# Performance work log

Hardware: AMD Instinct MI355X
Metric: run time of the kernel (lower is better)

## Reference

```python
import jax, jax.numpy as jnp
import numpy as np
from jax import lax

FEAT_STRIDE = 16
PRE_NMS_TOP_N = 6000   # cfg['TEST'].RPN_PRE_NMS_TOP_N
POST_NMS_TOP_N = 300   # cfg['TEST'].RPN_POST_NMS_TOP_N
NMS_THRESH = 0.7       # cfg['TEST'].RPN_NMS_THRESH
MIN_SIZE = 16.0        # cfg['TEST'].RPN_MIN_SIZE
B, A, H, W = 32, 9, 128, 128
NEG_INF = jnp.float32(-1e30)


def _whctrs(a):
    w = a[2] - a[0] + 1.0
    h = a[3] - a[1] + 1.0
    return w, h, a[0] + 0.5 * (w - 1), a[1] + 0.5 * (h - 1)

def _mkanchors(ws, hs, xc, yc):
    ws = ws[:, None]; hs = hs[:, None]
    return np.hstack((xc - 0.5 * (ws - 1), yc - 0.5 * (hs - 1),
                      xc + 0.5 * (ws - 1), yc + 0.5 * (hs - 1)))

def _ratio_enum(anchor, ratios):
    w, h, xc, yc = _whctrs(anchor)
    size = w * h
    ws = np.round(np.sqrt(size / ratios))
    hs = np.round(ws * ratios)
    return _mkanchors(ws, hs, xc, yc)

def _scale_enum(anchor, scales):
    w, h, xc, yc = _whctrs(anchor)
    return _mkanchors(w * scales, h * scales, xc, yc)

def generate_anchors(base_size=16, ratios=np.array([0.5, 1.0, 2.0]), scales=np.array([8.0, 16.0, 32.0])):
    base = np.array([1, 1, base_size, base_size], dtype=np.float64) - 1
    ra = _ratio_enum(base, ratios)
    return np.vstack([_scale_enum(ra[i], scales) for i in range(ra.shape[0])]).astype(np.float32)

_BASE_ANCHORS = generate_anchors()  # (A, 4)

def _all_anchors(h, w):
    sx = np.arange(w) * FEAT_STRIDE
    sy = np.arange(h) * FEAT_STRIDE
    sx, sy = np.meshgrid(sx, sy)  # row-major (h, w) matches permute(0,2,3,1) ordering
    shifts = np.stack([sx.ravel(), sy.ravel(), sx.ravel(), sy.ravel()], axis=1).astype(np.float32)
    return jnp.asarray((shifts[:, None, :] + _BASE_ANCHORS[None, :, :]).reshape(-1, 4))  # (h*w*A, 4)

# ---- bbox_transform_inv / clip_boxes ----

def _decode(anchors, deltas):
    ws = anchors[:, 2] - anchors[:, 0] + 1.0
    hs = anchors[:, 3] - anchors[:, 1] + 1.0
    cx = anchors[:, 0] + 0.5 * ws
    cy = anchors[:, 1] + 0.5 * hs
    dx, dy, dw, dh = deltas[:, 0], deltas[:, 1], deltas[:, 2], deltas[:, 3]
    pcx = dx * ws + cx
    pcy = dy * hs + cy
    pw = jnp.exp(dw) * ws
    ph = jnp.exp(dh) * hs
    return jnp.stack([pcx - 0.5 * pw, pcy - 0.5 * ph, pcx + 0.5 * pw, pcy + 0.5 * ph], axis=1)

def _clip(b, imh, imw):
    x1 = jnp.clip(b[:, 0], 0.0, imw - 1.0)
    y1 = jnp.clip(b[:, 1], 0.0, imh - 1.0)
    x2 = jnp.clip(b[:, 2], 0.0, imw - 1.0)
    y2 = jnp.clip(b[:, 3], 0.0, imh - 1.0)
    return jnp.stack([x1, y1, x2, y2], axis=1)

# ---- greedy NMS: pick top-score box, suppress IoU > thresh, repeat POST times ----

def _nms_select(boxes, scores):
    # boxes: (PRE, 4) score-sorted; scores: (PRE,)
    areas = (boxes[:, 2] - boxes[:, 0] + 1.0) * (boxes[:, 3] - boxes[:, 1] + 1.0)

    def body(i, st):
        s, keep, valid = st
        j = jnp.argmax(s)
        keep = keep.at[i].set(j)
        valid = valid.at[i].set(s[j] > NEG_INF)
        b = boxes[j]
        xx1 = jnp.maximum(b[0], boxes[:, 0])
        yy1 = jnp.maximum(b[1], boxes[:, 1])
        xx2 = jnp.minimum(b[2], boxes[:, 2])
        yy2 = jnp.minimum(b[3], boxes[:, 3])
        inter = jnp.maximum(xx2 - xx1 + 1.0, 0.0) * jnp.maximum(yy2 - yy1 + 1.0, 0.0)
        iou = inter / jnp.maximum(areas[j] + areas - inter, 1e-6)
        s = jnp.where(iou > NMS_THRESH, NEG_INF, s)  # suppresses j itself (IoU = 1)
        return s, keep, valid

    init = (scores, jnp.zeros((POST_NMS_TOP_N,), jnp.int32), jnp.zeros((POST_NMS_TOP_N,), bool))
    _, keep, valid = lax.fori_loop(0, POST_NMS_TOP_N, body, init)
    return keep, valid

def _per_image(sc, dl, info, anchors):
    prop = _clip(_decode(anchors, dl), info[0], info[1])  # (K*A, 4)
    ws = prop[:, 2] - prop[:, 0] + 1.0
    hs = prop[:, 3] - prop[:, 1] + 1.0
    min_sz = MIN_SIZE * info[2]
    sc = jnp.where((ws >= min_sz) & (hs >= min_sz), sc, NEG_INF)
    top_s, top_i = lax.top_k(sc, PRE_NMS_TOP_N)
    cand = prop[top_i]  # (PRE, 4)
    keep, valid = _nms_select(cand, top_s)
    return cand[keep] * valid[:, None].astype(cand.dtype)  # zero-pad invalid rows

def _forward(rpn_cls_prob, rpn_bbox_pred, im_info):
    b, _, h, w = rpn_cls_prob.shape
    anchors = _all_anchors(h, w)
    scores = rpn_cls_prob[:, A:, :, :].transpose(0, 2, 3, 1).reshape(b, -1)  # (b, h*w*A)
    deltas = rpn_bbox_pred.transpose(0, 2, 3, 1).reshape(b, -1, 4)           # (b, h*w*A, 4)
    boxes = jax.vmap(lambda s, d, i: _per_image(s, d, i, anchors))(scores, deltas, im_info)
    ids = jnp.broadcast_to(jnp.arange(b, dtype=boxes.dtype)[:, None, None], (b, POST_NMS_TOP_N, 1))
    return jnp.concatenate([ids, boxes], axis=2)  # (b, POST, 5): [batch_idx, x1, y1, x2, y2]

def setup_inputs() -> dict:
    key = jax.random.key(0)
    k1, k2 = jax.random.split(key)
    rpn_cls_prob = jax.random.uniform(k1, (B, 2 * A, H, W), dtype=jnp.float32)
    rpn_bbox_pred = jax.random.normal(k2, (B, 4 * A, H, W), dtype=jnp.float32) * 0.2
    im_info = jnp.tile(jnp.array([[H * FEAT_STRIDE, W * FEAT_STRIDE, 1.0]], dtype=jnp.float32), (B, 1))
    return {"rpn_cls_prob": rpn_cls_prob, "rpn_bbox_pred": rpn_bbox_pred, "im_info": im_info}

def reference(rpn_cls_prob, rpn_bbox_pred, im_info):
    return _forward(rpn_cls_prob, rpn_bbox_pred, im_info)
```

## Files before the change

kernel.cpp:

```cpp
#include <hip/hip_runtime.h>
#include <cstdint>
#include <cstddef>

#pragma clang fp contract(off)

typedef unsigned long long u64;

#define NB 32
#define NA 9
#define NH 128
#define NW 128
#define HW (NH*NW)
#define NANCH (NA*HW)
#define PRE_N 6000
#define POST_N 300
#define CAND_CAP 8192
#define NMS_T 0.7f
#define GX_GATHER 24

__constant__ float c_wa[9] = {184.f,368.f,736.f,128.f,256.f,512.f,88.f,176.f,352.f};
__constant__ float c_ha[9] = {96.f,192.f,384.f,128.f,256.f,512.f,176.f,352.f,704.f};

__device__ __forceinline__ float4 decode_clip(int a, int h, int w,
    float dx, float dy, float dlw, float dlh, float imh, float imw) {
  float wa = c_wa[a], ha = c_ha[a];
  float cx = (float)w * 16.0f + 8.0f;
  float cy = (float)h * 16.0f + 8.0f;
  float pcx = dx * wa + cx;
  float pcy = dy * ha + cy;
  float pw = expf(dlw) * wa;
  float ph = expf(dlh) * ha;
  float x1 = pcx - 0.5f * pw;
  float y1 = pcy - 0.5f * ph;
  float x2 = pcx + 0.5f * pw;
  float y2 = pcy + 0.5f * ph;
  float4 r;
  r.x = fminf(fmaxf(x1, 0.0f), imw - 1.0f);
  r.y = fminf(fmaxf(y1, 0.0f), imh - 1.0f);
  r.z = fminf(fmaxf(x2, 0.0f), imw - 1.0f);
  r.w = fminf(fmaxf(y2, 0.0f), imh - 1.0f);
  return r;
}

__device__ __forceinline__ unsigned score_key(float sc, float bw, float bh, float msz) {
  unsigned bits = __float_as_uint(sc);
  unsigned key = (bits & 0x80000000u) ? ~bits : (bits | 0x80000000u);
  if (!(bw >= msz && bh >= msz)) key = 0u;
  return key;
}

__device__ __forceinline__ bool sup_test4(float4 v, float ar, float4 p, float pa) {
  float xx1 = fmaxf(p.x, v.x), yy1 = fmaxf(p.y, v.y);
  float xx2 = fminf(p.z, v.z), yy2 = fminf(p.w, v.w);
  float iw = fmaxf(xx2 - xx1 + 1.0f, 0.0f);
  float ih = fmaxf(yy2 - yy1 + 1.0f, 0.0f);
  float inter = iw * ih;
  float iou = inter / fmaxf(pa + ar - inter, 1e-6f);
  return iou > NMS_T;
}

__global__ __launch_bounds__(256) void k_keys(const float* __restrict__ cls,
    const float* __restrict__ dl, const float* __restrict__ info,
    unsigned* __restrict__ keys, unsigned* __restrict__ hist) {
  __shared__ unsigned hsh[4096];
  int tid = threadIdx.x;
  for (int i = tid; i < 4096; i += 256) hsh[i] = 0;
  int t = blockIdx.x * 256 + tid;
  int b = blockIdx.y;
  int hw0 = t * 4;
  int h = hw0 >> 7;
  const float* dlb  = dl  + (size_t)b * (4*NA*HW);
  const float* clsb = cls + (size_t)b * (2*NA*HW);
  float imh = info[b*3+0], imw = info[b*3+1];
  float msz = 16.0f * info[b*3+2];
  unsigned* kb = keys + (size_t)b * NANCH;
  __syncthreads();
  #pragma unroll
  for (int a = 0; a < 9; ++a) {
    float4 dx4 = *(const float4*)&dlb[(a*4+0)*HW + hw0];
    float4 dy4 = *(const float4*)&dlb[(a*4+1)*HW + hw0];
    float4 dw4 = *(const float4*)&dlb[(a*4+2)*HW + hw0];
    float4 dh4 = *(const float4*)&dlb[(a*4+3)*HW + hw0];
    float4 sc4 = *(const float4*)&clsb[(NA+a)*HW + hw0];
    uint4 out;
    {
      float4 bx = decode_clip(a, h, (hw0+0)&127, dx4.x, dy4.x, dw4.x, dh4.x, imh, imw);
      out.x = score_key(sc4.x, bx.z-bx.x+1.0f, bx.w-bx.y+1.0f, msz);
    }
    {
      float4 bx = decode_clip(a, h, (hw0+1)&127, dx4.y, dy4.y, dw4.y, dh4.y, imh, imw);
      out.y = score_key(sc4.y, bx.z-bx.x+1.0f, bx.w-bx.y+1.0f, msz);
    }
    {
      float4 bx = decode_clip(a, h, (hw0+2)&127, dx4.z, dy4.z, dw4.z, dh4.z, imh, imw);
      out.z = score_key(sc4.z, bx.z-bx.x+1.0f, bx.w-bx.y+1.0f, msz);
    }
    {
      float4 bx = decode_clip(a, h, (hw0+3)&127, dx4.w, dy4.w, dw4.w, dh4.w, imh, imw);
      out.w = score_key(sc4.w, bx.z-bx.x+1.0f, bx.w-bx.y+1.0f, msz);
    }
    *(uint4*)&kb[a*HW + hw0] = out;
    atomicAdd(&hsh[out.x >> 20], 1u);
    atomicAdd(&hsh[out.y >> 20], 1u);
    atomicAdd(&hsh[out.z >> 20], 1u);
    atomicAdd(&hsh[out.w >> 20], 1u);
  }
  __syncthreads();
  unsigned* gb = hist + ((size_t)b << 12);
  for (int i = tid; i < 4096; i += 256) {
    unsigned v = hsh[i];
    if (v) atomicAdd(&gb[i], v);
  }
}

__global__ __launch_bounds__(256) void k_select1(const unsigned* __restrict__ hist,
                                                 unsigned* __restrict__ selA) {
  int b = blockIdx.x, tid = threadIdx.x;
  const unsigned* hb = hist + ((size_t)b << 12);
  __shared__ unsigned part[256];
  unsigned s = 0;
  for (int i = 0; i < 16; ++i) s += hb[tid*16 + i];
  part[tid] = s;
  __syncthreads();
  for (int off = 1; off < 256; off <<= 1) {
    unsigned v = (tid + off < 256) ? part[tid + off] : 0u;
    __syncthreads();
    part[tid] += v;
    __syncthreads();
  }
  unsigned St = part[tid];
  unsigned Sn = (tid < 255) ? part[tid + 1] : 0u;
  if (St >= (unsigned)PRE_N && Sn < (unsigned)PRE_N) {
    unsigned cum = Sn, B = 0, cumAbove = Sn;
    for (int i = 15; i >= 0; --i) {
      unsigned v = hb[tid*16 + i];
      if (cum + v >= (unsigned)PRE_N) { B = (unsigned)(tid*16 + i); cumAbove = cum; break; }
      cum += v;
    }
    selA[b*2+0] = B;
    selA[b*2+1] = cumAbove;
  }
}

__global__ __launch_bounds__(256) void k_hist2(const unsigned* __restrict__ keys,
    const unsigned* __restrict__ selA, unsigned* __restrict__ hist2) {
  __shared__ unsigned h[4096];
  int b = blockIdx.y, tid = threadIdx.x;
  for (int i = tid; i < 4096; i += 256) h[i] = 0;
  __syncthreads();
  unsigned B = selA[b*2+0];
  const unsigned* kb = keys + (size_t)b * NANCH;
  for (int i = blockIdx.x * 256 + tid; i < NANCH; i += gridDim.x * 256) {
    unsigned k = kb[i];
    if ((k >> 20) == B) atomicAdd(&h[(k >> 8) & 4095u], 1u);
  }
  __syncthreads();
  unsigned* gb = hist2 + ((size_t)b << 12);
  for (int i = tid; i < 4096; i += 256) { unsigned v = h[i]; if (v) atomicAdd(&gb[i], v); }
}

__global__ __launch_bounds__(256) void k_select2(const unsigned* __restrict__ hist2,
    const unsigned* __restrict__ selA, unsigned* __restrict__ thr) {
  int b = blockIdx.x, tid = threadIdx.x;
  const unsigned* hb = hist2 + ((size_t)b << 12);
  unsigned B = selA[b*2+0], cum0 = selA[b*2+1];
  __shared__ unsigned part[256];
  unsigned s = 0;
  for (int i = 0; i < 16; ++i) s += hb[tid*16 + i];
  part[tid] = s;
  __syncthreads();
  for (int off = 1; off < 256; off <<= 1) {
    unsigned v = (tid + off < 256) ? part[tid + off] : 0u;
    __syncthreads();
    part[tid] += v;
    __syncthreads();
  }
  unsigned St = cum0 + part[tid];
  unsigned Sn = cum0 + ((tid < 255) ? part[tid + 1] : 0u);
  if (St >= (unsigned)PRE_N && Sn < (unsigned)PRE_N) {
    unsigned cum = Sn, t = 1u;
    for (int i = 15; i >= 0; --i) {
      unsigned v = hb[tid*16 + i];
      if (cum + v >= (unsigned)PRE_N) {
        t = (B << 20) | ((unsigned)(tid*16 + i) << 8);
        break;
      }
      cum += v;
    }
    if (t == 0u) t = 1u;
    thr[b] = t;
  }
}

__global__ __launch_bounds__(256) void k_gather(const unsigned* __restrict__ keys,
    const unsigned* __restrict__ thr, unsigned* __restrict__ cnt,
    u64* __restrict__ cand) {
  int b = blockIdx.y, tid = threadIdx.x;
  int lane = tid & 63, wv = tid >> 6;
  __shared__ unsigned wcnt[4], woff[4], blkbase;
  unsigned t_ = thr[b];
  const unsigned* kb = keys + (size_t)b * NANCH;
  u64* cb = cand + (size_t)b * CAND_CAP;
  unsigned* cp = cnt + (size_t)b * 64;
  const int PER_BLK = NANCH / GX_GATHER;
  int base0 = blockIdx.x * PER_BLK;
  for (int it = 0; it < PER_BLK / 256; ++it) {
    int j = base0 + it * 256 + tid;
    unsigned key = kb[j];
    bool pass = key >= t_;
    u64 mask = __ballot(pass);
    if (lane == 0) wcnt[wv] = (unsigned)__popcll(mask);
    __syncthreads();
    if (tid == 0) {
      unsigned s0 = 0;
      for (int w = 0; w < 4; ++w) { woff[w] = s0; s0 += wcnt[w]; }
      blkbase = s0 ? atomicAdd(cp, s0) : 0u;
    }
    __syncthreads();
    if (pass) {
      unsigned pos = blkbase + woff[wv] + (unsigned)__popcll(mask & ((1ull << lane) - 1ull));
      if (pos < CAND_CAP) {
        int a = j >> 14, hw = j & (HW - 1);
        unsigned oi = (unsigned)(hw * 9 + a);
        cb[pos] = ((u64)key << 32) | (unsigned)(~oi);
      }
    }
    __syncthreads();
  }
}


__global__ __launch_bounds__(256) void k_sortA(u64* __restrict__ cand) {
  __shared__ u64 sm[1024];
  int blk = blockIdx.x;
  int b = blk >> 3, c = blk & 7;
  u64* cb = cand + (size_t)b * CAND_CAP + (size_t)c * 1024;
  int tid = threadIdx.x;
  for (int t = tid; t < 1024; t += 256) sm[t] = cb[t];
  bool blkdesc = (c & 1) == 0;
  for (int k = 2; k <= 1024; k <<= 1) {
    for (int j = k >> 1; j > 0; j >>= 1) {
      __syncthreads();
      for (int t = tid; t < 1024; t += 256) {
        int p = t ^ j;
        if (p > t) {
          bool up = (k == 1024) ? blkdesc : ((t & k) == 0);
          u64 x = sm[t], y = sm[p];
          if (up ? (x < y) : (x > y)) { sm[t] = y; sm[p] = x; }
        }
      }
    }
  }
  __syncthreads();
  for (int t = tid; t < 1024; t += 256) cb[t] = sm[t];
}

template<int SIZE, int THREADS>
__global__ __launch_bounds__(THREADS) void k_merge(u64* __restrict__ cand) {
  __shared__ u64 sm[SIZE];
  const int nblk = CAND_CAP / SIZE;
  int blk = blockIdx.x;
  int b = blk / nblk, m = blk % nblk;
  u64* cb = cand + (size_t)b * CAND_CAP + (size_t)m * SIZE;
  int tid = threadIdx.x;
  for (int t = tid; t < SIZE; t += THREADS) sm[t] = cb[t];
  bool desc = (m & 1) == 0;
  for (int j = SIZE >> 1; j > 0; j >>= 1) {
    __syncthreads();
    for (int t = tid; t < SIZE; t += THREADS) {
      int p = t ^ j;
      if (p > t) {
        u64 x = sm[t], y = sm[p];
        if (desc ? (x < y) : (x > y)) { sm[t] = y; sm[p] = x; }
      }
    }
  }
  __syncthreads();
  for (int t = tid; t < SIZE; t += THREADS) cb[t] = sm[t];
}

__global__ __launch_bounds__(1024) void k_sortF(u64* __restrict__ cand,
    const float* __restrict__ dl, const float* __restrict__ info,
    float4* __restrict__ boxes) {
  __shared__ u64 sm[CAND_CAP];
  int b = blockIdx.x, tid = threadIdx.x;
  u64* cb = cand + (size_t)b * CAND_CAP;
  for (int t = tid; t < CAND_CAP; t += 1024) sm[t] = cb[t];
  for (int j = CAND_CAP >> 1; j > 0; j >>= 1) {
    __syncthreads();
    for (int t = tid; t < CAND_CAP; t += 1024) {
      int p = t ^ j;
      if (p > t) {
        u64 x = sm[t], y = sm[p];
        if (x < y) { sm[t] = y; sm[p] = x; }
      }
    }
  }
  __syncthreads();
  const float* dlb = dl + (size_t)b * (4*NA*HW);
  float imh = info[b*3+0], imw = info[b*3+1];
  for (int t = tid; t < PRE_N; t += 1024) {
    u64 ck = sm[t];
    cb[t] = ck;
    float4 bx = make_float4(0.f, 0.f, 0.f, 0.f);
    if ((unsigned)(ck >> 32) != 0u) {
      int i = (int)(~(unsigned)(ck & 0xFFFFFFFFull));
      int a = i % 9, hw = i / 9;
      int h = hw >> 7, w = hw & 127;
      bx = decode_clip(a, h, w,
                       dlb[(a*4+0)*HW + hw], dlb[(a*4+1)*HW + hw],
                       dlb[(a*4+2)*HW + hw], dlb[(a*4+3)*HW + hw], imh, imw);
    }
    boxes[(size_t)b * PRE_N + t] = bx;
  }
}

__global__ __launch_bounds__(1024) void k_nms(const u64* __restrict__ cand,
    const float4* __restrict__ boxes, float* __restrict__ out) {
  int b = blockIdx.x, tid = threadIdx.x;
  int c = tid & 255, seg = tid >> 8;
  int lane = tid & 63, wv = tid >> 6;
  int cg = c >> 6;
  __shared__ float4 kbox[POST_N];
  __shared__ float  karea[POST_N];
  __shared__ float4 cbox[256];
  __shared__ float  carea[256];
  __shared__ unsigned supf[256];
  __shared__ u64 sup[256][4];
  __shared__ u64 aliveM[4];
  __shared__ u64 kgW[4];
  __shared__ int s_nk;
  if (tid == 0) s_nk = 0;
  __syncthreads();
  const u64* cb = cand + (size_t)b * CAND_CAP;
  const float4* bb = boxes + (size_t)b * PRE_N;
  float* ob = out + (size_t)b * (POST_N * 5);
  volatile unsigned* svf = supf;

  for (int base = 0; base < PRE_N; base += 256) {
    if (tid < 256) {
      int i = base + tid;
      u64 ck = (i < PRE_N) ? cb[i] : 0ull;
      bool valid = (unsigned)(ck >> 32) != 0u;
      float4 v = valid ? bb[i] : make_float4(0.f, 0.f, 0.f, 0.f);
      cbox[tid] = v;
      carea[tid] = (v.z - v.x + 1.0f) * (v.w - v.y + 1.0f);
      supf[tid] = valid ? 0u : 1u;
    }
    __syncthreads();
    int nk0 = s_nk;

    if (supf[c] == 0u) {
      float4 v = cbox[c]; float ar = carea[c];
      for (int k = seg; k < nk0; k += 4) {
        if (svf[c]) break;
        if (sup_test4(v, ar, kbox[k], karea[k])) { atomicOr(&supf[c], 1u); break; }
      }
    }
    __syncthreads();

    if (seg == 0) {
      u64 am = __ballot(supf[c] == 0u);
      if (lane == 0) aliveM[wv] = am;
    }
    __syncthreads();

    if (supf[c] == 0u && seg <= cg) {
      float4 v = cbox[c]; float ar = carea[c];
      u64 m = aliveM[seg];
      if (seg == cg) m &= (1ull << (c & 63)) - 1ull;
      u64 r = 0;
      while (m) {
        int j = __builtin_ctzll(m);
        m &= m - 1;
        int col = seg * 64 + j;
        if (sup_test4(v, ar, cbox[col], carea[col])) r |= 1ull << j;
      }
      sup[c][seg] = r;
    }
    __syncthreads();

    if (wv == 0) {
      u64 kw0 = 0, kw1 = 0, kw2 = 0, kw3 = 0;
      {
        bool a = (aliveM[0] >> lane) & 1;
        u64 r = a ? sup[lane][0] : 0;
        u64 cm = __ballot(a), kg = 0;
        while (cm) {
          int j = __builtin_ctzll(cm);
          kg |= 1ull << j;
          u64 rem = __ballot((r >> j) & 1);
          cm &= ~(rem | (1ull << j));
        }
        kw0 = kg;
      }
      {
        int cc = 64 + lane;
        bool a = (aliveM[1] >> lane) & 1;
        if (a) a = (sup[cc][0] & kw0) == 0;
        u64 r = a ? sup[cc][1] : 0;
        u64 cm = __ballot(a), kg = 0;
        while (cm) {
          int j = __builtin_ctzll(cm);
          kg |= 1ull << j;
          u64 rem = __ballot((r >> j) & 1);
          cm &= ~(rem | (1ull << j));
        }
        kw1 = kg;
      }
      {
        int cc = 128 + lane;
        bool a = (aliveM[2] >> lane) & 1;
        if (a) a = ((sup[cc][0] & kw0) == 0) && ((sup[cc][1] & kw1) == 0);
        u64 r = a ? sup[cc][2] : 0;
        u64 cm = __ballot(a), kg = 0;
        while (cm) {
          int j = __builtin_ctzll(cm);
          kg |= 1ull << j;
          u64 rem = __ballot((r >> j) & 1);
          cm &= ~(rem | (1ull << j));
        }
        kw2 = kg;
      }
      {
        int cc = 192 + lane;
        bool a = (aliveM[3] >> lane) & 1;
        if (a) a = ((sup[cc][0] & kw0) == 0) && ((sup[cc][1] & kw1) == 0) &&
                   ((sup[cc][2] & kw2) == 0);
        u64 r = a ? sup[cc][3] : 0;
        u64 cm = __ballot(a), kg = 0;
        while (cm) {
          int j = __builtin_ctzll(cm);
          kg |= 1ull << j;
          u64 rem = __ballot((r >> j) & 1);
          cm &= ~(rem | (1ull << j));
        }
        kw3 = kg;
      }
      if (lane == 0) { kgW[0] = kw0; kgW[1] = kw1; kgW[2] = kw2; kgW[3] = kw3; }
    }
    __syncthreads();

    if (tid < 256) {
      u64 kgw = kgW[wv];
      bool kept = (kgw >> lane) & 1;
      int pre = 0;
      for (int g = 0; g < wv; ++g) pre += (int)__popcll(kgW[g]);
      pre += (int)__popcll(kgw & ((1ull << lane) - 1ull));
      int rank = s_nk + pre;
      if (kept && rank < POST_N) {
        float4 v = cbox[tid];
        kbox[rank] = v; karea[rank] = carea[tid];
        ob[rank*5+0] = (float)b;
        ob[rank*5+1] = v.x; ob[rank*5+2] = v.y; ob[rank*5+3] = v.z; ob[rank*5+4] = v.w;
      }
    }
    __syncthreads();
    if (tid == 0) {
      int tot = (int)(__popcll(kgW[0]) + __popcll(kgW[1]) + __popcll(kgW[2]) + __popcll(kgW[3]));
      int nn = s_nk + tot;
      s_nk = nn < POST_N ? nn : POST_N;
    }
    __syncthreads();
    if (s_nk >= POST_N) break;
  }
  __syncthreads();
  int nk = s_nk;
  for (int r = nk + tid; r < POST_N; r += 1024) {
    ob[r*5+0] = (float)b;
    ob[r*5+1] = 0.f; ob[r*5+2] = 0.f; ob[r*5+3] = 0.f; ob[r*5+4] = 0.f;
  }
}

extern "C" void kernel_launch(void* const* d_in, const int* in_sizes, int n_in,
                              void* d_out, int out_size, void* d_ws, size_t ws_size,
                              hipStream_t stream) {
  const float* cls  = (const float*)d_in[0];
  const float* dl   = (const float*)d_in[1];
  const float* info = (const float*)d_in[2];
  float* out = (float*)d_out;
  char* ws = (char*)d_ws;

  const size_t OFF_KEYS = 0;
  const size_t OFF_H1   = 18874368;
  const size_t OFF_H2   = 19398656;
  const size_t OFF_SELA = 19922944;
  const size_t OFF_THR  = 19923200;
  const size_t OFF_CNT  = 19923328;
  const size_t OFF_CAND = 19931520;
  const size_t OFF_BOX  = 22028672;
  const size_t WS_NEED  = 25100672;
  if (ws_size < WS_NEED) return;

  unsigned* keys  = (unsigned*)(ws + OFF_KEYS);
  unsigned* h1    = (unsigned*)(ws + OFF_H1);
  unsigned* h2    = (unsigned*)(ws + OFF_H2);
  unsigned* selA  = (unsigned*)(ws + OFF_SELA);
  unsigned* thr   = (unsigned*)(ws + OFF_THR);
  unsigned* cnt   = (unsigned*)(ws + OFF_CNT);
  u64* cand = (u64*)(ws + OFF_CAND);
  float4* boxes   = (float4*)(ws + OFF_BOX);

  hipMemsetAsync(ws + OFF_H1, 0, OFF_BOX - OFF_H1, stream);

  dim3 g1(HW / 1024, NB);
  k_keys<<<g1, 256, 0, stream>>>(cls, dl, info, keys, h1);
  k_select1<<<NB, 256, 0, stream>>>(h1, selA);
  dim3 gh(8, NB);
  k_hist2<<<gh, 256, 0, stream>>>(keys, selA, h2);
  k_select2<<<NB, 256, 0, stream>>>(h2, selA, thr);
  dim3 gg(GX_GATHER, NB);
  k_gather<<<gg, 256, 0, stream>>>(keys, thr, cnt, cand);
  k_sortA<<<NB * 8, 256, 0, stream>>>(cand);
  k_merge<2048, 256><<<NB * 4, 256, 0, stream>>>(cand);
  k_merge<4096, 512><<<NB * 2, 512, 0, stream>>>(cand);
  k_sortF<<<NB, 1024, 0, stream>>>(cand, dl, info, boxes);
  k_nms<<<NB, 1024, 0, stream>>>(cand, boxes, out);
}
```

Measured before the change: 392.0 us.

## Fuse select kernels into consumers, restructure sort stages, split key grid by anchor

The two threshold-selection kernels are folded into the histogram and gather kernels, which each recompute the prefix scan from the histograms, removing launches and the selA/thr buffers. k_keys now launches one block per anchor slice for more parallelism. The bitonic sort is restructured: sortA handles 2048-element chunks, zero-fills beyond the candidate count and replaces the two merge kernels, and sortF runs the remaining merge stages. The memset no longer clears the candidate buffer. NMS skips fully suppressed chunks and drops a barrier using a snapshot count nk0, whose definition sits in lines not shown.

```diff
diff --git a/kernel.cpp b/kernel.cpp
--- a/kernel.cpp
+++ b/kernel.cpp
@@ -59,65 +59,9 @@
   return iou > NMS_T;
 }
 
-__global__ __launch_bounds__(256) void k_keys(const float* __restrict__ cls,
-    const float* __restrict__ dl, const float* __restrict__ info,
-    unsigned* __restrict__ keys, unsigned* __restrict__ hist) {
-  __shared__ unsigned hsh[4096];
+__device__ void find_B(const unsigned* __restrict__ hb, unsigned* part,
+                       unsigned* outB, unsigned* outCum) {
   int tid = threadIdx.x;
-  for (int i = tid; i < 4096; i += 256) hsh[i] = 0;
-  int t = blockIdx.x * 256 + tid;
-  int b = blockIdx.y;
-  int hw0 = t * 4;
-  int h = hw0 >> 7;
-  const float* dlb  = dl  + (size_t)b * (4*NA*HW);
-  const float* clsb = cls + (size_t)b * (2*NA*HW);
-  float imh = info[b*3+0], imw = info[b*3+1];
-  float msz = 16.0f * info[b*3+2];
-  unsigned* kb = keys + (size_t)b * NANCH;
-  __syncthreads();
-  #pragma unroll
-  for (int a = 0; a < 9; ++a) {
-    float4 dx4 = *(const float4*)&dlb[(a*4+0)*HW + hw0];
-    float4 dy4 = *(const float4*)&dlb[(a*4+1)*HW + hw0];
-    float4 dw4 = *(const float4*)&dlb[(a*4+2)*HW + hw0];
-    float4 dh4 = *(const float4*)&dlb[(a*4+3)*HW + hw0];
-    float4 sc4 = *(const float4*)&clsb[(NA+a)*HW + hw0];
-    uint4 out;
-    {
-      float4 bx = decode_clip(a, h, (hw0+0)&127, dx4.x, dy4.x, dw4.x, dh4.x, imh, imw);
-      out.x = score_key(sc4.x, bx.z-bx.x+1.0f, bx.w-bx.y+1.0f, msz);
-    }
-    {
-      float4 bx = decode_clip(a, h, (hw0+1)&127, dx4.y, dy4.y, dw4.y, dh4.y, imh, imw);
-      out.y = score_key(sc4.y, bx.z-bx.x+1.0f, bx.w-bx.y+1.0f, msz);
-    }
-    {
-      float4 bx = decode_clip(a, h, (hw0+2)&127, dx4.z, dy4.z, dw4.z, dh4.z, imh, imw);
-      out.z = score_key(sc4.z, bx.z-bx.x+1.0f, bx.w-bx.y+1.0f, msz);
-    }
-    {
-      float4 bx = decode_clip(a, h, (hw0+3)&127, dx4.w, dy4.w, dw4.w, dh4.w, imh, imw);
-      out.w = score_key(sc4.w, bx.z-bx.x+1.0f, bx.w-bx.y+1.0f, msz);
-    }
-    *(uint4*)&kb[a*HW + hw0] = out;
-    atomicAdd(&hsh[out.x >> 20], 1u);
-    atomicAdd(&hsh[out.y >> 20], 1u);
-    atomicAdd(&hsh[out.z >> 20], 1u);
-    atomicAdd(&hsh[out.w >> 20], 1u);
-  }
-  __syncthreads();
-  unsigned* gb = hist + ((size_t)b << 12);
-  for (int i = tid; i < 4096; i += 256) {
-    unsigned v = hsh[i];
-    if (v) atomicAdd(&gb[i], v);
-  }
-}
-
-__global__ __launch_bounds__(256) void k_select1(const unsigned* __restrict__ hist,
-                                                 unsigned* __restrict__ selA) {
-  int b = blockIdx.x, tid = threadIdx.x;
-  const unsigned* hb = hist + ((size_t)b << 12);
-  __shared__ unsigned part[256];
   unsigned s = 0;
   for (int i = 0; i < 16; ++i) s += hb[tid*16 + i];
   part[tid] = s;
@@ -137,36 +81,16 @@
       if (cum + v >= (unsigned)PRE_N) { B = (unsigned)(tid*16 + i); cumAbove = cum; break; }
       cum += v;
     }
-    selA[b*2+0] = B;
-    selA[b*2+1] = cumAbove;
-  }
-}
-
-__global__ __launch_bounds__(256) void k_hist2(const unsigned* __restrict__ keys,
-    const unsigned* __restrict__ selA, unsigned* __restrict__ hist2) {
-  __shared__ unsigned h[4096];
-  int b = blockIdx.y, tid = threadIdx.x;
-  for (int i = tid; i < 4096; i += 256) h[i] = 0;
-  __syncthreads();
-  unsigned B = selA[b*2+0];
-  const unsigned* kb = keys + (size_t)b * NANCH;
-  for (int i = blockIdx.x * 256 + tid; i < NANCH; i += gridDim.x * 256) {
-    unsigned k = kb[i];
-    if ((k >> 20) == B) atomicAdd(&h[(k >> 8) & 4095u], 1u);
-  }
-  __syncthreads();
-  unsigned* gb = hist2 + ((size_t)b << 12);
-  for (int i = tid; i < 4096; i += 256) { unsigned v = h[i]; if (v) atomicAdd(&gb[i], v); }
-}
-
-__global__ __launch_bounds__(256) void k_select2(const unsigned* __restrict__ hist2,
-    const unsigned* __restrict__ selA, unsigned* __restrict__ thr) {
-  int b = blockIdx.x, tid = threadIdx.x;
-  const unsigned* hb = hist2 + ((size_t)b << 12);
-  unsigned B = selA[b*2+0], cum0 = selA[b*2+1];
-  __shared__ unsigned part[256];
+    *outB = B; *outCum = cumAbove;
+  }
+  __syncthreads();
+}
+
+__device__ void find_thr(const unsigned* __restrict__ hb2, unsigned B, unsigned cum0,
+                         unsigned* part, unsigned* outThr) {
+  int tid = threadIdx.x;
   unsigned s = 0;
-  for (int i = 0; i < 16; ++i) s += hb[tid*16 + i];
+  for (int i = 0; i < 16; ++i) s += hb2[tid*16 + i];
   part[tid] = s;
   __syncthreads();
   for (int off = 1; off < 256; off <<= 1) {
@@ -180,7 +104,7 @@
   if (St >= (unsigned)PRE_N && Sn < (unsigned)PRE_N) {
     unsigned cum = Sn, t = 1u;
     for (int i = 15; i >= 0; --i) {
-      unsigned v = hb[tid*16 + i];
+      unsigned v = hb2[tid*16 + i];
       if (cum + v >= (unsigned)PRE_N) {
         t = (B << 20) | ((unsigned)(tid*16 + i) << 8);
         break;
@@ -188,17 +112,95 @@
       cum += v;
     }
     if (t == 0u) t = 1u;
-    thr[b] = t;
-  }
+    *outThr = t;
+  }
+  __syncthreads();
+}
+
+__global__ __launch_bounds__(256) void k_keys(const float* __restrict__ cls,
+    const float* __restrict__ dl, const float* __restrict__ info,
+    unsigned* __restrict__ keys, unsigned* __restrict__ hist) {
+  __shared__ unsigned hsh[4096];
+  int tid = threadIdx.x;
+  for (int i = tid; i < 4096; i += 256) hsh[i] = 0;
+  int a = blockIdx.y, b = blockIdx.z;
+  int t = blockIdx.x * 256 + tid;
+  int hw0 = t * 4;
+  int h = hw0 >> 7;
+  const float* dlb  = dl  + (size_t)b * (4*NA*HW);
+  const float* clsb = cls + (size_t)b * (2*NA*HW);
+  float imh = info[b*3+0], imw = info[b*3+1];
+  float msz = 16.0f * info[b*3+2];
+  unsigned* kb = keys + (size_t)b * NANCH;
+  __syncthreads();
+  float4 dx4 = *(const float4*)&dlb[(a*4+0)*HW + hw0];
+  float4 dy4 = *(const float4*)&dlb[(a*4+1)*HW + hw0];
+  float4 dw4 = *(const float4*)&dlb[(a*4+2)*HW + hw0];
+  float4 dh4 = *(const float4*)&dlb[(a*4+3)*HW + hw0];
+  float4 sc4 = *(const float4*)&clsb[(NA+a)*HW + hw0];
+  uint4 out;
+  {
+    float4 bx = decode_clip(a, h, (hw0+0)&127, dx4.x, dy4.x, dw4.x, dh4.x, imh, imw);
+    out.x = score_key(sc4.x, bx.z-bx.x+1.0f, bx.w-bx.y+1.0f, msz);
+  }
+  {
+    float4 bx = decode_clip(a, h, (hw0+1)&127, dx4.y, dy4.y, dw4.y, dh4.y, imh, imw);
+    out.y = score_key(sc4.y, bx.z-bx.x+1.0f, bx.w-bx.y+1.0f, msz);
+  }
+  {
+    float4 bx = decode_clip(a, h, (hw0+2)&127, dx4.z, dy4.z, dw4.z, dh4.z, imh, imw);
+    out.z = score_key(sc4.z, bx.z-bx.x+1.0f, bx.w-bx.y+1.0f, msz);
+  }
+  {
+    float4 bx = decode_clip(a, h, (hw0+3)&127, dx4.w, dy4.w, dw4.w, dh4.w, imh, imw);
+    out.w = score_key(sc4.w, bx.z-bx.x+1.0f, bx.w-bx.y+1.0f, msz);
+  }
+  *(uint4*)&kb[a*HW + hw0] = out;
+  atomicAdd(&hsh[out.x >> 20], 1u);
+  atomicAdd(&hsh[out.y >> 20], 1u);
+  atomicAdd(&hsh[out.z >> 20], 1u);
+  atomicAdd(&hsh[out.w >> 20], 1u);
+  __syncthreads();
+  unsigned* gb = hist + ((size_t)b << 12);
+  for (int i = tid; i < 4096; i += 256) {
+    unsigned v = hsh[i];
+    if (v) atomicAdd(&gb[i], v);
+  }
+}
+
+__global__ __launch_bounds__(256) void k_hist2(const unsigned* __restrict__ keys,
+    const unsigned* __restrict__ hist1, unsigned* __restrict__ hist2) {
+  __shared__ unsigned h[4096];
+  __shared__ unsigned part[256];
+  __shared__ unsigned sB, sCum;
+  int b = blockIdx.y, tid = threadIdx.x;
+  for (int i = tid; i < 4096; i += 256) h[i] = 0;
+  __syncthreads();
+  find_B(hist1 + ((size_t)b << 12), part, &sB, &sCum);
+  unsigned B = sB;
+  const unsigned* kb = keys + (size_t)b * NANCH;
+  for (int i = blockIdx.x * 256 + tid; i < NANCH; i += gridDim.x * 256) {
+    unsigned k = kb[i];
+    if ((k >> 20) == B) atomicAdd(&h[(k >> 8) & 4095u], 1u);
+  }
+  __syncthreads();
+  unsigned* gb = hist2 + ((size_t)b << 12);
+  for (int i = tid; i < 4096; i += 256) { unsigned v = h[i]; if (v) atomicAdd(&gb[i], v); }
 }
 
 __global__ __launch_bounds__(256) void k_gather(const unsigned* __restrict__ keys,
-    const unsigned* __restrict__ thr, unsigned* __restrict__ cnt,
-    u64* __restrict__ cand) {
+    const unsigned* __restrict__ hist1, const unsigned* __restrict__ hist2,
+    unsigned* __restrict__ cnt, u64* __restrict__ cand) {
   int b = blockIdx.y, tid = threadIdx.x;
   int lane = tid & 63, wv = tid >> 6;
+  __shared__ unsigned part[256];
+  __shared__ unsigned sB, sCum, sThr;
   __shared__ unsigned wcnt[4], woff[4], blkbase;
-  unsigned t_ = thr[b];
+  if (tid == 0) sThr = 1u;
+  __syncthreads();
+  find_B(hist1 + ((size_t)b << 12), part, &sB, &sCum);
+  find_thr(hist2 + ((size_t)b << 12), sB, sCum, part, &sThr);
+  unsigned t_ = sThr;
   const unsigned* kb = keys + (size_t)b * NANCH;
   u64* cb = cand + (size_t)b * CAND_CAP;
   unsigned* cp = cnt + (size_t)b * 64;
@@ -229,22 +231,26 @@
   }
 }
 
-
-__global__ __launch_bounds__(256) void k_sortA(u64* __restrict__ cand) {
-  __shared__ u64 sm[1024];
+__global__ __launch_bounds__(256) void k_sortA(u64* __restrict__ cand,
+                                               const unsigned* __restrict__ cnt) {
+  __shared__ u64 sm[2048];
   int blk = blockIdx.x;
-  int b = blk >> 3, c = blk & 7;
-  u64* cb = cand + (size_t)b * CAND_CAP + (size_t)c * 1024;
+  int b = blk >> 2, c = blk & 3;
+  unsigned effcnt = cnt[b * 64];
+  if (effcnt > CAND_CAP) effcnt = CAND_CAP;
+  u64* cb = cand + (size_t)b * CAND_CAP + (size_t)c * 2048;
+  int base = c * 2048;
   int tid = threadIdx.x;
-  for (int t = tid; t < 1024; t += 256) sm[t] = cb[t];
+  for (int t = tid; t < 2048; t += 256)
+    sm[t] = ((unsigned)(base + t) < effcnt) ? cb[t] : 0ull;
   bool blkdesc = (c & 1) == 0;
-  for (int k = 2; k <= 1024; k <<= 1) {
+  for (int k = 2; k <= 2048; k <<= 1) {
     for (int j = k >> 1; j > 0; j >>= 1) {
       __syncthreads();
-      for (int t = tid; t < 1024; t += 256) {
+      for (int t = tid; t < 2048; t += 256) {
         int p = t ^ j;
         if (p > t) {
-          bool up = (k == 1024) ? blkdesc : ((t & k) == 0);
+          bool up = (k == 2048) ? blkdesc : ((t & k) == 0);
           u64 x = sm[t], y = sm[p];
           if (up ? (x < y) : (x > y)) { sm[t] = y; sm[p] = x; }
         }
@@ -252,31 +258,7 @@
     }
   }
   __syncthreads();
-  for (int t = tid; t < 1024; t += 256) cb[t] = sm[t];
-}
-
-template<int SIZE, int THREADS>
-__global__ __launch_bounds__(THREADS) void k_merge(u64* __restrict__ cand) {
-  __shared__ u64 sm[SIZE];
-  const int nblk = CAND_CAP / SIZE;
-  int blk = blockIdx.x;
-  int b = blk / nblk, m = blk % nblk;
-  u64* cb = cand + (size_t)b * CAND_CAP + (size_t)m * SIZE;
-  int tid = threadIdx.x;
-  for (int t = tid; t < SIZE; t += THREADS) sm[t] = cb[t];
-  bool desc = (m & 1) == 0;
-  for (int j = SIZE >> 1; j > 0; j >>= 1) {
-    __syncthreads();
-    for (int t = tid; t < SIZE; t += THREADS) {
-      int p = t ^ j;
-      if (p > t) {
-        u64 x = sm[t], y = sm[p];
-        if (desc ? (x < y) : (x > y)) { sm[t] = y; sm[p] = x; }
-      }
-    }
-  }
-  __syncthreads();
-  for (int t = tid; t < SIZE; t += THREADS) cb[t] = sm[t];
+  for (int t = tid; t < 2048; t += 256) cb[t] = sm[t];
 }
 
 __global__ __launch_bounds__(1024) void k_sortF(u64* __restrict__ cand,
@@ -286,13 +268,16 @@
   int b = blockIdx.x, tid = threadIdx.x;
   u64* cb = cand + (size_t)b * CAND_CAP;
   for (int t = tid; t < CAND_CAP; t += 1024) sm[t] = cb[t];
-  for (int j = CAND_CAP >> 1; j > 0; j >>= 1) {
-    __syncthreads();
-    for (int t = tid; t < CAND_CAP; t += 1024) {
-      int p = t ^ j;
-      if (p > t) {
-        u64 x = sm[t], y = sm[p];
-        if (x < y) { sm[t] = y; sm[p] = x; }
+  for (int k = 4096; k <= CAND_CAP; k <<= 1) {
+    for (int j = k >> 1; j > 0; j >>= 1) {
+      __syncthreads();
+      for (int t = tid; t < CAND_CAP; t += 1024) {
+        int p = t ^ j;
+        if (p > t) {
+          bool desc = (k == CAND_CAP) ? true : ((t & k) == 0);
+          u64 x = sm[t], y = sm[p];
+          if (desc ? (x < y) : (x > y)) { sm[t] = y; sm[p] = x; }
+        }
       }
     }
   }
@@ -364,6 +349,7 @@
       if (lane == 0) aliveM[wv] = am;
     }
     __syncthreads();
+    if ((aliveM[0] | aliveM[1] | aliveM[2] | aliveM[3]) == 0ull) continue;
 
     if (supf[c] == 0u && seg <= cg) {
       float4 v = cbox[c]; float ar = carea[c];
@@ -447,7 +433,7 @@
       int pre = 0;
       for (int g = 0; g < wv; ++g) pre += (int)__popcll(kgW[g]);
       pre += (int)__popcll(kgw & ((1ull << lane) - 1ull));
-      int rank = s_nk + pre;
+      int rank = nk0 + pre;
       if (kept && rank < POST_N) {
         float4 v = cbox[tid];
         kbox[rank] = v; karea[rank] = carea[tid];
@@ -455,10 +441,9 @@
         ob[rank*5+1] = v.x; ob[rank*5+2] = v.y; ob[rank*5+3] = v.z; ob[rank*5+4] = v.w;
       }
     }
-    __syncthreads();
     if (tid == 0) {
       int tot = (int)(__popcll(kgW[0]) + __popcll(kgW[1]) + __popcll(kgW[2]) + __popcll(kgW[3]));
-      int nn = s_nk + tot;
+      int nn = nk0 + tot;
       s_nk = nn < POST_N ? nn : POST_N;
     }
     __syncthreads();
@@ -484,36 +469,28 @@
   const size_t OFF_KEYS = 0;
   const size_t OFF_H1   = 18874368;
   const size_t OFF_H2   = 19398656;
-  const size_t OFF_SELA = 19922944;
-  const size_t OFF_THR  = 19923200;
-  const size_t OFF_CNT  = 19923328;
-  const size_t OFF_CAND = 19931520;
-  const size_t OFF_BOX  = 22028672;
-  const size_t WS_NEED  = 25100672;
+  const size_t OFF_CNT  = 19922944;
+  const size_t OFF_CAND = 19931136;
+  const size_t OFF_BOX  = 22028288;
+  const size_t WS_NEED  = 25100288;
   if (ws_size < WS_NEED) return;
 
   unsigned* keys  = (unsigned*)(ws + OFF_KEYS);
   unsigned* h1    = (unsigned*)(ws + OFF_H1);
   unsigned* h2    = (unsigned*)(ws + OFF_H2);
-  unsigned* selA  = (unsigned*)(ws + OFF_SELA);
-  unsigned* thr   = (unsigned*)(ws + OFF_THR);
   unsigned* cnt   = (unsigned*)(ws + OFF_CNT);
   u64* cand = (u64*)(ws + OFF_CAND);
   float4* boxes   = (float4*)(ws + OFF_BOX);
 
-  hipMemsetAsync(ws + OFF_H1, 0, OFF_BOX - OFF_H1, stream);
-
-  dim3 g1(HW / 1024, NB);
+  hipMemsetAsync(ws + OFF_H1, 0, OFF_CAND - OFF_H1, stream);
+
+  dim3 g1(16, NA, NB);
   k_keys<<<g1, 256, 0, stream>>>(cls, dl, info, keys, h1);
-  k_select1<<<NB, 256, 0, stream>>>(h1, selA);
   dim3 gh(8, NB);
-  k_hist2<<<gh, 256, 0, stream>>>(keys, selA, h2);
-  k_select2<<<NB, 256, 0, stream>>>(h2, selA, thr);
+  k_hist2<<<gh, 256, 0, stream>>>(keys, h1, h2);
   dim3 gg(GX_GATHER, NB);
-  k_gather<<<gg, 256, 0, stream>>>(keys, thr, cnt, cand);
-  k_sortA<<<NB * 8, 256, 0, stream>>>(cand);
-  k_merge<2048, 256><<<NB * 4, 256, 0, stream>>>(cand);
-  k_merge<4096, 512><<<NB * 2, 512, 0, stream>>>(cand);
+  k_gather<<<gg, 256, 0, stream>>>(keys, h1, h2, cnt, cand);
+  k_sortA<<<NB * 4, 256, 0, stream>>>(cand, cnt);
   k_sortF<<<NB, 1024, 0, stream>>>(cand, dl, info, boxes);
   k_nms<<<NB, 1024, 0, stream>>>(cand, boxes, out);
 }
```

Result: slower. 409.4 us (+4.4%).
